# Kernel optimization log

Measured on AMD Instinct MI355X. Metric: run time of the kernel, lower is better.

The kernel has to match this reference:

```python
import jax, jax.numpy as jnp
import numpy as np

N, C, H, W = 32, 512, 64, 64
R = 16
CB = C // R  # bottleneck channels = 32
EPS = 1e-5


def setup_inputs() -> dict:
    key = jax.random.key(0)
    ks = jax.random.split(key, 5)
    return {
        "x": jax.random.normal(ks[0], (N, C, H, W), dtype=jnp.float32),
        "wk_w": jax.random.normal(ks[1], (C,), dtype=jnp.float32) * (1.0 / np.sqrt(C)),
        "wk_b": jax.random.normal(ks[2], (1,), dtype=jnp.float32) * 0.01,
        "wv1_w": jax.random.normal(ks[3], (CB, C), dtype=jnp.float32) * (1.0 / np.sqrt(C)),
        "ln_g": jnp.ones((CB,), dtype=jnp.float32),
        "ln_b": jnp.zeros((CB,), dtype=jnp.float32),
        "wv2_w": jax.random.normal(ks[4], (C, CB), dtype=jnp.float32) * (1.0 / np.sqrt(CB)),
    }


def reference(x, wk_w, wk_b, wv1_w, ln_g, ln_b, wv2_w):
    # x: (n, c, h, w)
    # attention logits via 1x1 conv (c -> 1): (n, h, w)
    logits = jnp.einsum("nchw,c->nhw", x, wk_w) + wk_b[0]
    # Faithful to original: F.softmax(dim=2) on (n,1,h,w) -> softmax over H only
    attn = jax.nn.softmax(logits, axis=1)  # (n, h, w)
    # context pooling: (n, c, hw) @ (n, hw, 1) -> (n, c)
    ctx = jnp.einsum("nchw,nhw->nc", x, attn)
    # bottleneck: conv1x1 (c -> c/r), LayerNorm over channel, ReLU, conv1x1 (c/r -> c)
    v = ctx @ wv1_w.T  # (n, c/r)
    mu = jnp.mean(v, axis=-1, keepdims=True)
    var = jnp.mean((v - mu) ** 2, axis=-1, keepdims=True)
    v = (v - mu) * jax.lax.rsqrt(var + EPS) * ln_g + ln_b
    v = jax.nn.relu(v)
    out = v @ wv2_w.T  # (n, c)
    return out[:, :, None, None] + x
```

## Files before the change

### kernel.cpp

```cpp
#include <hip/hip_runtime.h>

#define N 32
#define C 512
#define H 64
#define W 64
#define HW 4096
#define CB 32
#define CCH 16
#define NCHUNK 32
#define EPS 1e-5f

typedef float fvec4 __attribute__((ext_vector_type(4)));

__global__ __launch_bounds__(256) void k1_logits(
    const float* __restrict__ x, const float* __restrict__ wk_w,
    float* __restrict__ partial)
{
    const int tid   = threadIdx.x;
    const int chunk = blockIdx.x;
    const int n     = blockIdx.y;
    const int c0    = chunk * CCH;
    const float4* xb = (const float4*)(x + ((size_t)n * C + c0) * HW);
    float4 acc[4];
    #pragma unroll
    for (int i = 0; i < 4; ++i) acc[i] = make_float4(0.f, 0.f, 0.f, 0.f);
    #pragma unroll 4
    for (int c = 0; c < CCH; ++c) {
        const float wv = wk_w[c0 + c];
        #pragma unroll
        for (int i = 0; i < 4; ++i) {
            const float4 xv = xb[c * 1024 + i * 256 + tid];
            acc[i].x += xv.x * wv; acc[i].y += xv.y * wv;
            acc[i].z += xv.z * wv; acc[i].w += xv.w * wv;
        }
    }
    float4* pb = (float4*)(partial + ((size_t)n * NCHUNK + chunk) * HW);
    #pragma unroll
    for (int i = 0; i < 4; ++i) pb[i * 256 + tid] = acc[i];
}

__global__ __launch_bounds__(256) void k2_softmax(
    const float* __restrict__ partial, const float* __restrict__ wk_b,
    float* __restrict__ attn)
{
    const int tid  = threadIdx.x;
    const int lane = tid & 63;
    const int wid  = blockIdx.x * 4 + (tid >> 6);
    const int n = wid >> 6;
    const int w = wid & 63;
    float l = wk_b[0];
    #pragma unroll
    for (int ch = 0; ch < NCHUNK; ++ch)
        l += partial[((size_t)n * NCHUNK + ch) * HW + lane * W + w];
    float m = l;
    #pragma unroll
    for (int o = 32; o > 0; o >>= 1) m = fmaxf(m, __shfl_xor(m, o));
    const float e = __expf(l - m);
    float s = e;
    #pragma unroll
    for (int o = 32; o > 0; o >>= 1) s += __shfl_xor(s, o);
    attn[(size_t)n * HW + lane * W + w] = e / s;
}

__global__ __launch_bounds__(256) void k3_ctx(
    const float* __restrict__ x, const float* __restrict__ attn,
    float* __restrict__ ctx)
{
    const int tid   = threadIdx.x;
    const int chunk = blockIdx.x;
    const int n     = blockIdx.y;
    const int c0    = chunk * CCH;
    const float4* ar = (const float4*)(attn + (size_t)n * HW);
    const float4* xb = (const float4*)(x + ((size_t)n * C + c0) * HW);
    float4 av[4];
    #pragma unroll
    for (int i = 0; i < 4; ++i) av[i] = ar[i * 256 + tid];
    float s[CCH];
    #pragma unroll
    for (int c = 0; c < CCH; ++c) s[c] = 0.f;
    #pragma unroll 4
    for (int c = 0; c < CCH; ++c) {
        float t = 0.f;
        #pragma unroll
        for (int i = 0; i < 4; ++i) {
            const float4 xv = xb[c * 1024 + i * 256 + tid];
            t += xv.x * av[i].x + xv.y * av[i].y
               + xv.z * av[i].z + xv.w * av[i].w;
        }
        s[c] = t;
    }
    __shared__ float red[CCH][4];
    const int lane = tid & 63, wv = tid >> 6;
    #pragma unroll
    for (int c = 0; c < CCH; ++c) {
        float t = s[c];
        #pragma unroll
        for (int o = 32; o > 0; o >>= 1) t += __shfl_xor(t, o);
        if (lane == 0) red[c][wv] = t;
    }
    __syncthreads();
    if (tid < CCH) {
        ctx[(size_t)n * C + c0 + tid] =
            red[tid][0] + red[tid][1] + red[tid][2] + red[tid][3];
    }
}

__global__ __launch_bounds__(256) void k4_bottleneck(
    const float* __restrict__ ctx, const float* __restrict__ wv1_w,
    const float* __restrict__ ln_g, const float* __restrict__ ln_b,
    const float* __restrict__ wv2_w, float* __restrict__ out_vec)
{
    __shared__ float ctx_s[C];
    __shared__ float v_s[CB];
    const int tid = threadIdx.x;
    const int n   = blockIdx.x;
    ctx_s[tid]       = ctx[n * C + tid];
    ctx_s[tid + 256] = ctx[n * C + tid + 256];
    __syncthreads();
    {
        const int b = tid >> 3, sub = tid & 7;
        const float* wr = wv1_w + b * C;
        float s = 0.f;
        #pragma unroll 8
        for (int j = sub; j < C; j += 8) s += wr[j] * ctx_s[j];
        #pragma unroll
        for (int o = 4; o > 0; o >>= 1) s += __shfl_down(s, o, 8);
        if (sub == 0) v_s[b] = s;
    }
    __syncthreads();
    if (tid < CB) {
        const float val = v_s[tid];
        float sm = val, sq = val * val;
        #pragma unroll
        for (int o = 16; o > 0; o >>= 1) {
            sm += __shfl_xor(sm, o, 32);
            sq += __shfl_xor(sq, o, 32);
        }
        const float mu  = sm / CB;
        const float var = sq / CB - mu * mu;
        const float vh  = (val - mu) * rsqrtf(var + EPS) * ln_g[tid] + ln_b[tid];
        v_s[tid] = fmaxf(vh, 0.f);
    }
    __syncthreads();
    for (int c = tid; c < C; c += 256) {
        const float* w2 = wv2_w + c * CB;
        float a = 0.f;
        #pragma unroll
        for (int b = 0; b < CB; ++b) a += v_s[b] * w2[b];
        out_vec[n * C + c] = a;
    }
}

__global__ __launch_bounds__(256) void k5_add(
    const float* __restrict__ x, const float* __restrict__ out_vec,
    float* __restrict__ out)
{
    const int tid = threadIdx.x;
    const int nc  = blockIdx.x;
    const fvec4* xp = (const fvec4*)x + (size_t)nc * (HW / 4);
    fvec4*       op = (fvec4*)out     + (size_t)nc * (HW / 4);
    const float a = out_vec[nc];
    #pragma unroll
    for (int i = 0; i < 4; ++i) {
        const int idx = i * 256 + tid;
        fvec4 v = __builtin_nontemporal_load(xp + idx);
        v += a;
        __builtin_nontemporal_store(v, op + idx);
    }
}

extern "C" void kernel_launch(void* const* d_in, const int* in_sizes, int n_in,
                              void* d_out, int out_size, void* d_ws, size_t ws_size,
                              hipStream_t stream) {
    const float* x     = (const float*)d_in[0];
    const float* wk_w  = (const float*)d_in[1];
    const float* wk_b  = (const float*)d_in[2];
    const float* wv1_w = (const float*)d_in[3];
    const float* ln_g  = (const float*)d_in[4];
    const float* ln_b  = (const float*)d_in[5];
    const float* wv2_w = (const float*)d_in[6];
    float* out = (float*)d_out;

    float* ws      = (float*)d_ws;
    float* partial = ws;
    float* attn    = partial + (size_t)N * NCHUNK * HW;
    float* ctx     = attn + (size_t)N * HW;
    float* ovec    = ctx + (size_t)N * C;

    k1_logits<<<dim3(NCHUNK, N), 256, 0, stream>>>(x, wk_w, partial);
    k2_softmax<<<512, 256, 0, stream>>>(partial, wk_b, attn);
    k3_ctx<<<dim3(NCHUNK, N), 256, 0, stream>>>(x, attn, ctx);
    k4_bottleneck<<<32, 256, 0, stream>>>(ctx, wv1_w, ln_g, ln_b, wv2_w, ovec);
    k5_add<<<16384, 256, 0, stream>>>(x, ovec, out);
}
```

Measured before the change: 576.0 us.

## Fuse all stages into one persistent kernel with software grid barriers

New measurement: 1.165 ms. 102% more time.

```diff
diff --git a/kernel.cpp b/kernel.cpp
--- a/kernel.cpp
+++ b/kernel.cpp
@@ -2,170 +2,198 @@
 
 #define N 32
 #define C 512
-#define H 64
-#define W 64
 #define HW 4096
 #define CB 32
 #define CCH 16
 #define NCHUNK 32
 #define EPS 1e-5f
+#define NBLK 1024u
 
 typedef float fvec4 __attribute__((ext_vector_type(4)));
 
-__global__ __launch_bounds__(256) void k1_logits(
+__device__ __forceinline__ void grid_barrier(unsigned* cnt, unsigned* gen)
+{
+    __syncthreads();
+    if (threadIdx.x == 0) {
+        const unsigned g =
+            __hip_atomic_load(gen, __ATOMIC_ACQUIRE, __HIP_MEMORY_SCOPE_AGENT);
+        __threadfence();
+        const unsigned a = __hip_atomic_fetch_add(
+            cnt, 1u, __ATOMIC_ACQ_REL, __HIP_MEMORY_SCOPE_AGENT);
+        if (a == NBLK - 1u) {
+            __hip_atomic_store(cnt, 0u, __ATOMIC_RELAXED,
+                               __HIP_MEMORY_SCOPE_AGENT);
+            __hip_atomic_fetch_add(gen, 1u, __ATOMIC_RELEASE,
+                                   __HIP_MEMORY_SCOPE_AGENT);
+        } else {
+            while (__hip_atomic_load(gen, __ATOMIC_ACQUIRE,
+                                     __HIP_MEMORY_SCOPE_AGENT) == g)
+                __builtin_amdgcn_s_sleep(2);
+        }
+        __threadfence();
+    }
+    __syncthreads();
+}
+
+__global__ __launch_bounds__(256, 4) void fused(
     const float* __restrict__ x, const float* __restrict__ wk_w,
-    float* __restrict__ partial)
+    const float* __restrict__ wk_b, const float* __restrict__ wv1_w,
+    const float* __restrict__ ln_g, const float* __restrict__ ln_b,
+    const float* __restrict__ wv2_w, float* __restrict__ out,
+    float* __restrict__ partial, float* __restrict__ attn,
+    float* __restrict__ ctx, float* __restrict__ ovec,
+    unsigned* __restrict__ bar)
 {
+    __shared__ float smem[4224];
+    unsigned* cnt = bar;
+    unsigned* gen = bar + 1;
     const int tid   = threadIdx.x;
-    const int chunk = blockIdx.x;
-    const int n     = blockIdx.y;
+    const int b     = blockIdx.x;
+    const int n     = b >> 5;
+    const int chunk = b & 31;
     const int c0    = chunk * CCH;
     const float4* xb = (const float4*)(x + ((size_t)n * C + c0) * HW);
-    float4 acc[4];
-    #pragma unroll
-    for (int i = 0; i < 4; ++i) acc[i] = make_float4(0.f, 0.f, 0.f, 0.f);
-    #pragma unroll 4
-    for (int c = 0; c < CCH; ++c) {
-        const float wv = wk_w[c0 + c];
-        #pragma unroll
-        for (int i = 0; i < 4; ++i) {
-            const float4 xv = xb[c * 1024 + i * 256 + tid];
-            acc[i].x += xv.x * wv; acc[i].y += xv.y * wv;
-            acc[i].z += xv.z * wv; acc[i].w += xv.w * wv;
-        }
-    }
-    float4* pb = (float4*)(partial + ((size_t)n * NCHUNK + chunk) * HW);
-    #pragma unroll
-    for (int i = 0; i < 4; ++i) pb[i * 256 + tid] = acc[i];
-}
-
-__global__ __launch_bounds__(256) void k2_softmax(
-    const float* __restrict__ partial, const float* __restrict__ wk_b,
-    float* __restrict__ attn)
-{
-    const int tid  = threadIdx.x;
-    const int lane = tid & 63;
-    const int wid  = blockIdx.x * 4 + (tid >> 6);
-    const int n = wid >> 6;
-    const int w = wid & 63;
-    float l = wk_b[0];
-    #pragma unroll
-    for (int ch = 0; ch < NCHUNK; ++ch)
-        l += partial[((size_t)n * NCHUNK + ch) * HW + lane * W + w];
-    float m = l;
-    #pragma unroll
-    for (int o = 32; o > 0; o >>= 1) m = fmaxf(m, __shfl_xor(m, o));
-    const float e = __expf(l - m);
-    float s = e;
-    #pragma unroll
-    for (int o = 32; o > 0; o >>= 1) s += __shfl_xor(s, o);
-    attn[(size_t)n * HW + lane * W + w] = e / s;
-}
-
-__global__ __launch_bounds__(256) void k3_ctx(
-    const float* __restrict__ x, const float* __restrict__ attn,
-    float* __restrict__ ctx)
-{
-    const int tid   = threadIdx.x;
-    const int chunk = blockIdx.x;
-    const int n     = blockIdx.y;
-    const int c0    = chunk * CCH;
-    const float4* ar = (const float4*)(attn + (size_t)n * HW);
-    const float4* xb = (const float4*)(x + ((size_t)n * C + c0) * HW);
-    float4 av[4];
-    #pragma unroll
-    for (int i = 0; i < 4; ++i) av[i] = ar[i * 256 + tid];
-    float s[CCH];
-    #pragma unroll
-    for (int c = 0; c < CCH; ++c) s[c] = 0.f;
-    #pragma unroll 4
-    for (int c = 0; c < CCH; ++c) {
-        float t = 0.f;
-        #pragma unroll
-        for (int i = 0; i < 4; ++i) {
-            const float4 xv = xb[c * 1024 + i * 256 + tid];
-            t += xv.x * av[i].x + xv.y * av[i].y
-               + xv.z * av[i].z + xv.w * av[i].w;
-        }
-        s[c] = t;
-    }
-    __shared__ float red[CCH][4];
-    const int lane = tid & 63, wv = tid >> 6;
-    #pragma unroll
-    for (int c = 0; c < CCH; ++c) {
-        float t = s[c];
-        #pragma unroll
-        for (int o = 32; o > 0; o >>= 1) t += __shfl_xor(t, o);
-        if (lane == 0) red[c][wv] = t;
-    }
-    __syncthreads();
-    if (tid < CCH) {
-        ctx[(size_t)n * C + c0 + tid] =
-            red[tid][0] + red[tid][1] + red[tid][2] + red[tid][3];
-    }
-}
-
-__global__ __launch_bounds__(256) void k4_bottleneck(
-    const float* __restrict__ ctx, const float* __restrict__ wv1_w,
-    const float* __restrict__ ln_g, const float* __restrict__ ln_b,
-    const float* __restrict__ wv2_w, float* __restrict__ out_vec)
-{
-    __shared__ float ctx_s[C];
-    __shared__ float v_s[CB];
-    const int tid = threadIdx.x;
-    const int n   = blockIdx.x;
-    ctx_s[tid]       = ctx[n * C + tid];
-    ctx_s[tid + 256] = ctx[n * C + tid + 256];
-    __syncthreads();
+
     {
-        const int b = tid >> 3, sub = tid & 7;
-        const float* wr = wv1_w + b * C;
-        float s = 0.f;
-        #pragma unroll 8
-        for (int j = sub; j < C; j += 8) s += wr[j] * ctx_s[j];
-        #pragma unroll
-        for (int o = 4; o > 0; o >>= 1) s += __shfl_down(s, o, 8);
-        if (sub == 0) v_s[b] = s;
-    }
-    __syncthreads();
-    if (tid < CB) {
-        const float val = v_s[tid];
-        float sm = val, sq = val * val;
-        #pragma unroll
-        for (int o = 16; o > 0; o >>= 1) {
-            sm += __shfl_xor(sm, o, 32);
-            sq += __shfl_xor(sq, o, 32);
-        }
-        const float mu  = sm / CB;
-        const float var = sq / CB - mu * mu;
-        const float vh  = (val - mu) * rsqrtf(var + EPS) * ln_g[tid] + ln_b[tid];
-        v_s[tid] = fmaxf(vh, 0.f);
-    }
-    __syncthreads();
-    for (int c = tid; c < C; c += 256) {
-        const float* w2 = wv2_w + c * CB;
-        float a = 0.f;
-        #pragma unroll
-        for (int b = 0; b < CB; ++b) a += v_s[b] * w2[b];
-        out_vec[n * C + c] = a;
-    }
-}
-
-__global__ __launch_bounds__(256) void k5_add(
-    const float* __restrict__ x, const float* __restrict__ out_vec,
-    float* __restrict__ out)
-{
-    const int tid = threadIdx.x;
-    const int nc  = blockIdx.x;
-    const fvec4* xp = (const fvec4*)x + (size_t)nc * (HW / 4);
-    fvec4*       op = (fvec4*)out     + (size_t)nc * (HW / 4);
-    const float a = out_vec[nc];
-    #pragma unroll
-    for (int i = 0; i < 4; ++i) {
-        const int idx = i * 256 + tid;
-        fvec4 v = __builtin_nontemporal_load(xp + idx);
-        v += a;
-        __builtin_nontemporal_store(v, op + idx);
+        float4 acc[4];
+        #pragma unroll
+        for (int i = 0; i < 4; ++i) acc[i] = make_float4(0.f, 0.f, 0.f, 0.f);
+        #pragma unroll 4
+        for (int c = 0; c < CCH; ++c) {
+            const float wv = wk_w[c0 + c];
+            #pragma unroll
+            for (int i = 0; i < 4; ++i) {
+                const float4 xv = xb[c * 1024 + i * 256 + tid];
+                acc[i].x += xv.x * wv; acc[i].y += xv.y * wv;
+                acc[i].z += xv.z * wv; acc[i].w += xv.w * wv;
+            }
+        }
+        float4* pb = (float4*)(partial + ((size_t)n * NCHUNK + chunk) * HW);
+        #pragma unroll
+        for (int i = 0; i < 4; ++i) pb[i * 256 + tid] = acc[i];
+    }
+    grid_barrier(cnt, gen);
+
+    if (b < N) {
+        float* l_s  = smem;
+        float* m_s  = smem + 4096;
+        float* is_s = smem + 4160;
+        const float bias = wk_b[0];
+        for (int i4 = tid; i4 < 1024; i4 += 256) {
+            float4 sum = make_float4(bias, bias, bias, bias);
+            for (int ch = 0; ch < NCHUNK; ++ch) {
+                const float4 p = ((const float4*)(partial +
+                    ((size_t)b * NCHUNK + ch) * HW))[i4];
+                sum.x += p.x; sum.y += p.y; sum.z += p.z; sum.w += p.w;
+            }
+            ((float4*)l_s)[i4] = sum;
+        }
+        __syncthreads();
+        if (tid < 64) {
+            float m = -1e30f;
+            for (int h = 0; h < 64; ++h) m = fmaxf(m, l_s[h * 64 + tid]);
+            float s = 0.f;
+            for (int h = 0; h < 64; ++h) s += __expf(l_s[h * 64 + tid] - m);
+            m_s[tid] = m; is_s[tid] = 1.f / s;
+        }
+        __syncthreads();
+        for (int idx = tid; idx < HW; idx += 256) {
+            const int w = idx & 63;
+            attn[(size_t)b * HW + idx] = __expf(l_s[idx] - m_s[w]) * is_s[w];
+        }
+    }
+    grid_barrier(cnt, gen);
+
+    {
+        const float4* ar = (const float4*)(attn + (size_t)n * HW);
+        float4 av[4];
+        #pragma unroll
+        for (int i = 0; i < 4; ++i) av[i] = ar[i * 256 + tid];
+        float s[CCH];
+        #pragma unroll
+        for (int c = 0; c < CCH; ++c) s[c] = 0.f;
+        #pragma unroll 4
+        for (int c = CCH - 1; c >= 0; --c) {
+            float t = 0.f;
+            #pragma unroll
+            for (int i = 0; i < 4; ++i) {
+                const float4 xv = xb[c * 1024 + i * 256 + tid];
+                t += xv.x * av[i].x + xv.y * av[i].y
+                   + xv.z * av[i].z + xv.w * av[i].w;
+            }
+            s[c] = t;
+        }
+        const int lane = tid & 63, wv = tid >> 6;
+        #pragma unroll
+        for (int c = 0; c < CCH; ++c) {
+            float t = s[c];
+            #pragma unroll
+            for (int o = 32; o > 0; o >>= 1) t += __shfl_xor(t, o);
+            if (lane == 0) smem[c * 4 + wv] = t;
+        }
+        __syncthreads();
+        if (tid < CCH) {
+            ctx[(size_t)n * C + c0 + tid] = smem[tid * 4] + smem[tid * 4 + 1]
+                                          + smem[tid * 4 + 2] + smem[tid * 4 + 3];
+        }
+    }
+    grid_barrier(cnt, gen);
+
+    if (b < N) {
+        float* ctx_s = smem;
+        float* v_s   = smem + 512;
+        ctx_s[tid]       = ctx[b * C + tid];
+        ctx_s[tid + 256] = ctx[b * C + tid + 256];
+        __syncthreads();
+        {
+            const int bb = tid >> 3, sub = tid & 7;
+            const float* wr = wv1_w + bb * C;
+            float s = 0.f;
+            #pragma unroll 8
+            for (int j = sub; j < C; j += 8) s += wr[j] * ctx_s[j];
+            #pragma unroll
+            for (int o = 4; o > 0; o >>= 1) s += __shfl_down(s, o, 8);
+            if (sub == 0) v_s[bb] = s;
+        }
+        __syncthreads();
+        if (tid < CB) {
+            const float val = v_s[tid];
+            float sm = val, sq = val * val;
+            #pragma unroll
+            for (int o = 16; o > 0; o >>= 1) {
+                sm += __shfl_xor(sm, o, 32);
+                sq += __shfl_xor(sq, o, 32);
+            }
+            const float mu  = sm / CB;
+            const float var = sq / CB - mu * mu;
+            const float vh  = (val - mu) * rsqrtf(var + EPS) * ln_g[tid] + ln_b[tid];
+            v_s[tid] = fmaxf(vh, 0.f);
+        }
+        __syncthreads();
+        for (int c = tid; c < C; c += 256) {
+            const float* w2 = wv2_w + c * CB;
+            float a = 0.f;
+            #pragma unroll
+            for (int bq = 0; bq < CB; ++bq) a += v_s[bq] * w2[bq];
+            ovec[b * C + c] = a;
+        }
+    }
+    grid_barrier(cnt, gen);
+
+    {
+        const fvec4* xp = (const fvec4*)x   + ((size_t)n * C + c0) * 1024;
+        fvec4*       op = (fvec4*)out       + ((size_t)n * C + c0) * 1024;
+        #pragma unroll 4
+        for (int c = 0; c < CCH; ++c) {
+            const float a = ovec[n * C + c0 + c];
+            #pragma unroll
+            for (int i = 0; i < 4; ++i) {
+                const int idx = c * 1024 + i * 256 + tid;
+                fvec4 v = xp[idx];
+                v += a;
+                __builtin_nontemporal_store(v, op + idx);
+            }
+        }
     }
 }
 
@@ -186,10 +214,10 @@
     float* attn    = partial + (size_t)N * NCHUNK * HW;
     float* ctx     = attn + (size_t)N * HW;
     float* ovec    = ctx + (size_t)N * C;
-
-    k1_logits<<<dim3(NCHUNK, N), 256, 0, stream>>>(x, wk_w, partial);
-    k2_softmax<<<512, 256, 0, stream>>>(partial, wk_b, attn);
-    k3_ctx<<<dim3(NCHUNK, N), 256, 0, stream>>>(x, attn, ctx);
-    k4_bottleneck<<<32, 256, 0, stream>>>(ctx, wv1_w, ln_g, ln_b, wv2_w, ovec);
-    k5_add<<<16384, 256, 0, stream>>>(x, ovec, out);
+    unsigned* bar  = (unsigned*)(ovec + (size_t)N * C);
+
+    hipMemsetAsync(bar, 0, 2 * sizeof(unsigned), stream);
+
+    fused<<<NBLK, 256, 0, stream>>>(x, wk_w, wk_b, wv1_w, ln_g, ln_b, wv2_w,
+                                    out, partial, attn, ctx, ovec, bar);
 }
```
